# Performance work log

Hardware: AMD Instinct MI355X
Metric: run time of the kernel (lower is better)

The kernel has to match this reference:

```python
import jax, jax.numpy as jnp
import numpy as np

B, C, HEADS, W, Hh = 8, 512, 8, 32, 32
D = C // HEADS  # 64 per-head dim
N = W * Hh      # 1024 spatial tokens


def setup_inputs() -> dict:
    key = jax.random.key(0)
    ks = jax.random.split(key, 10)
    s = 1.0 / np.sqrt(C)
    return {
        "x": jax.random.normal(ks[0], (B, C, W, Hh), dtype=jnp.float32),
        "Wq": jax.random.normal(ks[1], (C, C), dtype=jnp.float32) * s,
        "bq": jax.random.normal(ks[2], (C,), dtype=jnp.float32) * 0.01,
        "Wk": jax.random.normal(ks[3], (C, C), dtype=jnp.float32) * s,
        "bk": jax.random.normal(ks[4], (C,), dtype=jnp.float32) * 0.01,
        "Wv": jax.random.normal(ks[5], (C, C), dtype=jnp.float32) * s,
        "bv": jax.random.normal(ks[6], (C,), dtype=jnp.float32) * 0.01,
        "rel_h": jax.random.normal(ks[7], (1, HEADS, D, 1, Hh), dtype=jnp.float32),
        "rel_w": jax.random.normal(ks[8], (1, HEADS, D, W, 1), dtype=jnp.float32),
    }


def reference(x, Wq, bq, Wk, bk, Wv, bv, rel_h, rel_w):
    b = x.shape[0]
    xf = x.reshape(b, C, N)  # [B, C, N] — 1x1 conv == per-position linear
    proj = lambda Wm, bm: (jnp.einsum('oc,bcn->bon', Wm, xf) + bm[None, :, None]).reshape(b, HEADS, D, N)
    q = proj(Wq, bq)  # [B, H, D, N]
    k = proj(Wk, bk)
    v = proj(Wv, bv)
    # content-content: q^T k -> [B, H, N, N]
    cc = jnp.einsum('bhdn,bhdm->bhnm', q, k)
    # relative position bias: (rel_h + rel_w) -> [H, D, N], then rel^T @ q
    rel = (rel_h + rel_w).reshape(HEADS, D, N)
    cp = jnp.einsum('hdn,bhdm->bhnm', rel, q)  # [B, H, N, N]
    attn = jax.nn.softmax(cc + cp, axis=-1)
    # out = v @ attn^T : out[d,m] = sum_n v[d,n] * attn[m,n]
    out = jnp.einsum('bhdn,bhmn->bhdm', v, attn)  # [B, H, D, N]
    return out.reshape(b, C, W, Hh)
```

## Files before the change

kernel.cpp:

```cpp
#include <hip/hip_runtime.h>

typedef _Float16 half8 __attribute__((ext_vector_type(8)));
typedef _Float16 half4 __attribute__((ext_vector_type(4)));
typedef float f32x4 __attribute__((ext_vector_type(4)));

__device__ __forceinline__ void glds16(const void* g, void* l) {
    __builtin_amdgcn_global_load_lds(
        (const __attribute__((address_space(1))) unsigned int*)g,
        (__attribute__((address_space(3))) unsigned int*)l, 16, 0, 0);
}


__global__ void k_prep_all(const float* __restrict__ Wq, const float* __restrict__ Wk,
                           const float* __restrict__ Wv, const float* __restrict__ bq,
                           const float* __restrict__ bk, const float* __restrict__ bv,
                           const float* __restrict__ x, const float* __restrict__ rel_h,
                           const float* __restrict__ rel_w, _Float16* __restrict__ Wf,
                           float* __restrict__ bias2, _Float16* __restrict__ xTf,
                           _Float16* __restrict__ rel2) {
    __shared__ float xs[64][65];
    int bid = blockIdx.x;
    if (bid < 384) {
        int t = bid * 256 + threadIdx.x;
        int m = t >> 6;
        int c8 = (t & 63) << 3;
        const float* src = (m < 512) ? (Wq + m * 512)
                         : (m < 1024 ? (Wk + (m - 512) * 512) : (Wv + (m - 1024) * 512));
        float4 v0 = *(const float4*)(src + c8);
        float4 v1 = *(const float4*)(src + c8 + 4);
        half8 o;
        o[0] = (_Float16)v0.x; o[1] = (_Float16)v0.y; o[2] = (_Float16)v0.z; o[3] = (_Float16)v0.w;
        o[4] = (_Float16)v1.x; o[5] = (_Float16)v1.y; o[6] = (_Float16)v1.z; o[7] = (_Float16)v1.w;
        *(half8*)(Wf + (size_t)m * 512 + c8) = o;
        if (t < 1536)
            bias2[t] = (t < 512) ? bq[t] : (t < 1024 ? bk[t - 512] : bv[t - 1024]);
    } else if (bid < 1408) {
        int i = bid - 384;
        int nt = (i & 15) << 6, ct = ((i >> 4) & 7) << 6, b = i >> 7;
        int t = threadIdx.x;
        const float* xb = x + ((size_t)b * 512 + ct) * 1024 + nt;
#pragma unroll
        for (int p = 0; p < 4; ++p) {
            int c = p * 16 + (t >> 4), n4 = (t & 15) * 4;
            float4 v = *(const float4*)(xb + (size_t)c * 1024 + n4);
            xs[c][n4] = v.x; xs[c][n4 + 1] = v.y; xs[c][n4 + 2] = v.z; xs[c][n4 + 3] = v.w;
        }
        __syncthreads();
        int nl = t >> 2, part = t & 3;
        _Float16* rowp = xTf + ((size_t)b * 1024 + nt + nl) * 512;
#pragma unroll
        for (int g = 0; g < 2; ++g) {
            half8 o;
#pragma unroll
            for (int j = 0; j < 8; ++j)
                o[j] = (_Float16)xs[part * 16 + g * 8 + j][nl];
            *(half8*)(rowp + ct + part * 16 + g * 8) = o;
        }
    } else {
        int tid = (bid - 1408) * 256 + threadIdx.x;
        int h = tid >> 13;
        int rem = tid & 8191;
        int n = rem >> 3;
        int g = rem & 7;
        int hh = n & 31, ww = n >> 5;
        half8 o;
#pragma unroll
        for (int j = 0; j < 8; ++j) {
            int d = g * 8 + j;
            o[j] = (_Float16)(rel_h[(h * 64 + d) * 32 + hh] + rel_w[(h * 64 + d) * 32 + ww]);
        }
        *(half8*)(rel2 + ((size_t)h * 1024 + n) * 64 + g * 8) = o;
    }
}

__global__ __launch_bounds__(256, 3) void k_proj(const _Float16* __restrict__ Wf,
                                                 const _Float16* __restrict__ xTf,
                                                 const float* __restrict__ bias2,
                                                 _Float16* __restrict__ q2,
                                                 _Float16* __restrict__ k2,
                                                 _Float16* __restrict__ vb) {
    __shared__ __align__(16) _Float16 As[8192];
    __shared__ __align__(16) _Float16 Bs[8192];
    int t = threadIdx.x;
    int lane = t & 63, w = t >> 6;
    int lm = lane & 15, lq = lane >> 4;
    int wr = (w >> 1) * 64, wc = (w & 1) * 64;
    int mb = blockIdx.y * 128, nb = blockIdx.x * 128, b = blockIdx.z;
    int rl = lane >> 2;
    int csw = ((lane & 3) ^ ((lane >> 3) & 3)) * 8;
    const _Float16* Ag0 = Wf + (size_t)(mb + w * 32 + rl) * 512 + csw;
    const _Float16* Ag1 = Ag0 + 16 * 512;
    const _Float16* Bg0 = xTf + ((size_t)b * 1024 + nb + w * 32 + rl) * 512 + csw;
    const _Float16* Bg1 = Bg0 + 16 * 512;
    f32x4 acc[4][4];
#pragma unroll
    for (int i = 0; i < 4; ++i)
#pragma unroll
        for (int j = 0; j < 4; ++j) acc[i][j] = {0.f, 0.f, 0.f, 0.f};
    int fsw = (lq ^ ((lm >> 1) & 3)) * 8;
    for (int k0 = 0; k0 < 512; k0 += 64) {
#pragma unroll
        for (int kh = 0; kh < 2; ++kh) {
            int ko = k0 + kh * 32;
            glds16(Ag0 + ko, &As[kh * 4096 + (w * 32) * 32]);
            glds16(Ag1 + ko, &As[kh * 4096 + (w * 32 + 16) * 32]);
            glds16(Bg0 + ko, &Bs[kh * 4096 + (w * 32) * 32]);
            glds16(Bg1 + ko, &Bs[kh * 4096 + (w * 32 + 16) * 32]);
        }
        __syncthreads();
#pragma unroll
        for (int kh = 0; kh < 2; ++kh) {
            half8 af[4], bfr[4];
#pragma unroll
            for (int mt = 0; mt < 4; ++mt)
                af[mt] = *(half8*)&As[kh * 4096 + (wr + mt * 16 + lm) * 32 + fsw];
#pragma unroll
            for (int nt = 0; nt < 4; ++nt)
                bfr[nt] = *(half8*)&Bs[kh * 4096 + (wc + nt * 16 + lm) * 32 + fsw];
#pragma unroll
            for (int mt = 0; mt < 4; ++mt)
#pragma unroll
                for (int nt = 0; nt < 4; ++nt)
                    acc[mt][nt] = __builtin_amdgcn_mfma_f32_16x16x32_f16(af[mt], bfr[nt], acc[mt][nt], 0, 0, 0);
        }
        __syncthreads();
    }
    int sect = mb >> 9;
    int hloc = ((mb & 511) + wr) >> 6;
    size_t bh = (size_t)b * 8 + hloc;
    if (sect < 2) {
        float sc = (sect == 0) ? 1.44269504089f : 1.0f;
        _Float16* dst = (sect == 0 ? q2 : k2) + bh * 1024 * 64;
#pragma unroll
        for (int mt = 0; mt < 4; ++mt) {
            int d0 = mt * 16 + lq * 4;
            float bi0 = bias2[mb + wr + d0];
            float bi1 = bias2[mb + wr + d0 + 1];
            float bi2 = bias2[mb + wr + d0 + 2];
            float bi3 = bias2[mb + wr + d0 + 3];
#pragma unroll
            for (int nt = 0; nt < 4; ++nt) {
                int n = nb + wc + nt * 16 + lm;
                half4 o;
                o[0] = (_Float16)((acc[mt][nt][0] + bi0) * sc);
                o[1] = (_Float16)((acc[mt][nt][1] + bi1) * sc);
                o[2] = (_Float16)((acc[mt][nt][2] + bi2) * sc);
                o[3] = (_Float16)((acc[mt][nt][3] + bi3) * sc);
                *(half4*)(dst + (size_t)n * 64 + d0) = o;
            }
        }
    } else {
        _Float16* dst = vb + bh * 64 * 1024;
#pragma unroll
        for (int mt = 0; mt < 4; ++mt)
#pragma unroll
            for (int reg = 0; reg < 4; ++reg) {
                int d = mt * 16 + lq * 4 + reg;
                float bi = bias2[mb + wr + d];
#pragma unroll
                for (int nt = 0; nt < 4; ++nt) {
                    int n = nb + wc + nt * 16 + lm;
                    dst[(size_t)d * 1024 + n] = (_Float16)(acc[mt][nt][reg] + bi);
                }
            }
    }
}

__global__ __launch_bounds__(256, 3) void k_attn(const _Float16* __restrict__ q2,
                                                 const _Float16* __restrict__ k2,
                                                 const _Float16* __restrict__ rel2,
                                                 const _Float16* __restrict__ vb,
                                                 float* __restrict__ out) {
    __shared__ __align__(16) char pool[45056];
    _Float16* kb_s = (_Float16*)pool;
    _Float16* v_s  = (_Float16*)(pool + 17408);
    _Float16* p_s  = (_Float16*)(pool + 26624);
    int t = threadIdx.x;
    int lane = t & 63, w = t >> 6;
    int lm = lane & 15, lq = lane >> 4;
    int lin = blockIdx.x;
    int mt0 = lin >> 6;
    int bh_ = lin & 63;
    int h = bh_ & 7, b = bh_ >> 3;
    size_t bh = (size_t)b * 8 + h;
    const _Float16* q2b = q2 + bh * 1024 * 64;
    const _Float16* k2b = k2 + bh * 1024 * 64;
    const _Float16* relb = rel2 + (size_t)h * 1024 * 64;
    const _Float16* vbb = vb + bh * 64 * 1024;
    float* outb = out + bh * 64 * 1024 + mt0 * 128;

    int r = t >> 2, part = t & 3;
    const _Float16* ksrc = ((part < 2) ? (k2b + part * 32) : (q2b + (part - 2) * 32));
    int vc = (t & 3) * 16;
    const _Float16* vsrcb = vbb + (size_t)r * 1024 + vc;
    _Float16* kdst = kb_s + r * 136 + part * 32;
    _Float16* vdst = v_s + r * 72 + vc;

    uint4 kc0, kc1, kc2, kc3, vv0, vv1;
    {
        const uint4* s_ = (const uint4*)(ksrc + (size_t)r * 64);
        kc0 = s_[0]; kc1 = s_[1]; kc2 = s_[2]; kc3 = s_[3];
        const uint4* v_ = (const uint4*)vsrcb;
        vv0 = v_[0]; vv1 = v_[1];
    }

    {
        int n = mt0 * 128 + r;
        const _Float16* src = (part < 2) ? (q2b + (size_t)n * 64 + part * 32)
                                         : (relb + (size_t)n * 64 + (part - 2) * 32);
        ((uint4*)kdst)[0] = ((const uint4*)src)[0];
        ((uint4*)kdst)[1] = ((const uint4*)src)[1];
        ((uint4*)kdst)[2] = ((const uint4*)src)[2];
        ((uint4*)kdst)[3] = ((const uint4*)src)[3];
    }
    __syncthreads();
    half8 ah0[4], ah1[4];
#pragma unroll
    for (int kk = 0; kk < 4; ++kk)
        ah0[kk] = *(half8*)&kb_s[(w * 16 + lm) * 136 + kk * 32 + lq * 8];
    __syncthreads();
    {
        int n = mt0 * 128 + 64 + r;
        const _Float16* src = (part < 2) ? (q2b + (size_t)n * 64 + part * 32)
                                         : (relb + (size_t)n * 64 + (part - 2) * 32);
        ((uint4*)kdst)[0] = ((const uint4*)src)[0];
        ((uint4*)kdst)[1] = ((const uint4*)src)[1];
        ((uint4*)kdst)[2] = ((const uint4*)src)[2];
        ((uint4*)kdst)[3] = ((const uint4*)src)[3];
    }
    __syncthreads();
#pragma unroll
    for (int kk = 0; kk < 4; ++kk)
        ah1[kk] = *(half8*)&kb_s[(w * 16 + lm) * 136 + kk * 32 + lq * 8];
    __syncthreads();

    f32x4 acco0[4], acco1[4];
#pragma unroll
    for (int i = 0; i < 4; ++i) { acco0[i] = {0.f, 0.f, 0.f, 0.f}; acco1[i] = {0.f, 0.f, 0.f, 0.f}; }
    float mrun0 = -3e38f, lrun0 = 0.f, mrun1 = -3e38f, lrun1 = 0.f;

    for (int kt = 0; kt < 16; ++kt) {
        ((uint4*)kdst)[0] = kc0;
        ((uint4*)kdst)[1] = kc1;
        ((uint4*)kdst)[2] = kc2;
        ((uint4*)kdst)[3] = kc3;
        ((uint4*)vdst)[0] = vv0;
        ((uint4*)vdst)[1] = vv1;
        __syncthreads();
        int nn = ((kt + 1) & 15) * 64;
        const uint4* s_ = (const uint4*)(ksrc + (size_t)(nn + r) * 64);
        uint4 kn0 = s_[0], kn1 = s_[1], kn2 = s_[2], kn3 = s_[3];
        const uint4* v_ = (const uint4*)(vsrcb + nn);
        uint4 vn0 = v_[0], vn1 = v_[1];
        f32x4 s0[4], s1[4];
#pragma unroll
        for (int ct = 0; ct < 4; ++ct) { s0[ct] = {0.f, 0.f, 0.f, 0.f}; s1[ct] = {0.f, 0.f, 0.f, 0.f}; }
#pragma unroll
        for (int ct = 0; ct < 4; ++ct) {
            half8 kf[4];
#pragma unroll
            for (int kk = 0; kk < 4; ++kk)
                kf[kk] = *(half8*)&kb_s[(ct * 16 + lm) * 136 + kk * 32 + lq * 8];
#pragma unroll
            for (int kk = 0; kk < 4; ++kk) {
                s0[ct] = __builtin_amdgcn_mfma_f32_16x16x32_f16(kf[kk], ah0[kk], s0[ct], 0, 0, 0);
                s1[ct] = __builtin_amdgcn_mfma_f32_16x16x32_f16(kf[kk], ah1[kk], s1[ct], 0, 0, 0);
            }
        }
        {
            float mx = -3e38f;
#pragma unroll
            for (int ct = 0; ct < 4; ++ct)
#pragma unroll
                for (int reg = 0; reg < 4; ++reg) mx = fmaxf(mx, s0[ct][reg]);
            mx = fmaxf(mx, __shfl_xor(mx, 16));
            mx = fmaxf(mx, __shfl_xor(mx, 32));
            float mnew = fmaxf(mrun0, mx);
            float al_ = exp2f(mrun0 - mnew);
            float rs = 0.f;
#pragma unroll
            for (int ct = 0; ct < 4; ++ct) {
                float p0 = exp2f(s0[ct][0] - mnew);
                float p1 = exp2f(s0[ct][1] - mnew);
                float p2 = exp2f(s0[ct][2] - mnew);
                float p3 = exp2f(s0[ct][3] - mnew);
                rs += (p0 + p1) + (p2 + p3);
                half4 o; o[0] = (_Float16)p0; o[1] = (_Float16)p1; o[2] = (_Float16)p2; o[3] = (_Float16)p3;
                *(half4*)&p_s[(w * 16 + lm) * 72 + ct * 16 + lq * 4] = o;
            }
            rs += __shfl_xor(rs, 16);
            rs += __shfl_xor(rs, 32);
            lrun0 = lrun0 * al_ + rs;
            mrun0 = mnew;
#pragma unroll
            for (int dt = 0; dt < 4; ++dt) {
                acco0[dt][0] *= al_; acco0[dt][1] *= al_;
                acco0[dt][2] *= al_; acco0[dt][3] *= al_;
            }
        }
        {
            float mx = -3e38f;
#pragma unroll
            for (int ct = 0; ct < 4; ++ct)
#pragma unroll
                for (int reg = 0; reg < 4; ++reg) mx = fmaxf(mx, s1[ct][reg]);
            mx = fmaxf(mx, __shfl_xor(mx, 16));
            mx = fmaxf(mx, __shfl_xor(mx, 32));
            float mnew = fmaxf(mrun1, mx);
            float al_ = exp2f(mrun1 - mnew);
            float rs = 0.f;
#pragma unroll
            for (int ct = 0; ct < 4; ++ct) {
                float p0 = exp2f(s1[ct][0] - mnew);
                float p1 = exp2f(s1[ct][1] - mnew);
                float p2 = exp2f(s1[ct][2] - mnew);
                float p3 = exp2f(s1[ct][3] - mnew);
                rs += (p0 + p1) + (p2 + p3);
                half4 o; o[0] = (_Float16)p0; o[1] = (_Float16)p1; o[2] = (_Float16)p2; o[3] = (_Float16)p3;
                *(half4*)&p_s[(64 + w * 16 + lm) * 72 + ct * 16 + lq * 4] = o;
            }
            rs += __shfl_xor(rs, 16);
            rs += __shfl_xor(rs, 32);
            lrun1 = lrun1 * al_ + rs;
            mrun1 = mnew;
#pragma unroll
            for (int dt = 0; dt < 4; ++dt) {
                acco1[dt][0] *= al_; acco1[dt][1] *= al_;
                acco1[dt][2] *= al_; acco1[dt][3] *= al_;
            }
        }
        half8 p0f[2], p1f[2];
#pragma unroll
        for (int ch = 0; ch < 2; ++ch) {
            p0f[ch] = *(half8*)&p_s[(w * 16 + lm) * 72 + ch * 32 + lq * 8];
            p1f[ch] = *(half8*)&p_s[(64 + w * 16 + lm) * 72 + ch * 32 + lq * 8];
        }
#pragma unroll
        for (int dt = 0; dt < 4; ++dt) {
            half8 vf0 = *(half8*)&v_s[(dt * 16 + lm) * 72 + lq * 8];
            half8 vf1 = *(half8*)&v_s[(dt * 16 + lm) * 72 + 32 + lq * 8];
            acco0[dt] = __builtin_amdgcn_mfma_f32_16x16x32_f16(vf0, p0f[0], acco0[dt], 0, 0, 0);
            acco0[dt] = __builtin_amdgcn_mfma_f32_16x16x32_f16(vf1, p0f[1], acco0[dt], 0, 0, 0);
            acco1[dt] = __builtin_amdgcn_mfma_f32_16x16x32_f16(vf0, p1f[0], acco1[dt], 0, 0, 0);
            acco1[dt] = __builtin_amdgcn_mfma_f32_16x16x32_f16(vf1, p1f[1], acco1[dt], 0, 0, 0);
        }
        __syncthreads();
        kc0 = kn0; kc1 = kn1; kc2 = kn2; kc3 = kn3;
        vv0 = vn0; vv1 = vn1;
    }
    float li0 = 1.f / lrun0, li1 = 1.f / lrun1;
#pragma unroll
    for (int dt = 0; dt < 4; ++dt)
#pragma unroll
        for (int reg = 0; reg < 4; ++reg) {
            int d = dt * 16 + lq * 4 + reg;
            outb[(size_t)d * 1024 + w * 16 + lm] = acco0[dt][reg] * li0;
            outb[(size_t)d * 1024 + 64 + w * 16 + lm] = acco1[dt][reg] * li1;
        }
}

extern "C" void kernel_launch(void* const* d_in, const int* in_sizes, int n_in,
                              void* d_out, int out_size, void* d_ws, size_t ws_size,
                              hipStream_t stream) {
    const float* x     = (const float*)d_in[0];
    const float* Wq    = (const float*)d_in[1];
    const float* bq    = (const float*)d_in[2];
    const float* Wk    = (const float*)d_in[3];
    const float* bk    = (const float*)d_in[4];
    const float* Wv    = (const float*)d_in[5];
    const float* bv    = (const float*)d_in[6];
    const float* rel_h = (const float*)d_in[7];
    const float* rel_w = (const float*)d_in[8];
    char* ws = (char*)d_ws;
    _Float16* Wf   = (_Float16*)(ws);
    float* bias2   = (float*)(ws + 1572864);
    _Float16* xTf  = (_Float16*)(ws + 1579008);
    _Float16* q2   = (_Float16*)(ws + 9967616);
    _Float16* k2   = (_Float16*)(ws + 18356224);
    _Float16* vb   = (_Float16*)(ws + 26744832);
    _Float16* rel2 = (_Float16*)(ws + 35133440);
    float* out = (float*)d_out;

    hipLaunchKernelGGL(k_prep_all, dim3(1664),     dim3(256), 0, stream,
                       Wq, Wk, Wv, bq, bk, bv, x, rel_h, rel_w, Wf, bias2, xTf, rel2);
    hipLaunchKernelGGL(k_proj,     dim3(8, 12, 8), dim3(256), 0, stream, Wf, xTf, bias2, q2, k2, vb);
    hipLaunchKernelGGL(k_attn,     dim3(512),      dim3(256), 0, stream, q2, k2, rel2, vb, out);
}
```

Before: 153.6 us.

## Fuse prep and projection kernels via persistent grid with global atomic barrier

Merges the input-conversion kernel and the QKV projection GEMM into one launch of 768 blocks. Each block first handles a grid-stride share of the prep work, then all blocks wait on a global atomic counter barrier before running the projection tile. This removes a kernel launch and its inter-kernel gap. In exchange it adds a memset per call and relies on all 768 blocks being co-resident (256 CUs × 3 blocks), otherwise the barrier deadlocks.

After: 262.2 us. 70.6% more time.

```diff
diff --git a/kernel.cpp b/kernel.cpp
--- a/kernel.cpp
+++ b/kernel.cpp
@@ -11,158 +11,176 @@
 }
 
 
-__global__ void k_prep_all(const float* __restrict__ Wq, const float* __restrict__ Wk,
-                           const float* __restrict__ Wv, const float* __restrict__ bq,
-                           const float* __restrict__ bk, const float* __restrict__ bv,
-                           const float* __restrict__ x, const float* __restrict__ rel_h,
-                           const float* __restrict__ rel_w, _Float16* __restrict__ Wf,
-                           float* __restrict__ bias2, _Float16* __restrict__ xTf,
-                           _Float16* __restrict__ rel2) {
-    __shared__ float xs[64][65];
-    int bid = blockIdx.x;
-    if (bid < 384) {
-        int t = bid * 256 + threadIdx.x;
-        int m = t >> 6;
-        int c8 = (t & 63) << 3;
-        const float* src = (m < 512) ? (Wq + m * 512)
-                         : (m < 1024 ? (Wk + (m - 512) * 512) : (Wv + (m - 1024) * 512));
-        float4 v0 = *(const float4*)(src + c8);
-        float4 v1 = *(const float4*)(src + c8 + 4);
-        half8 o;
-        o[0] = (_Float16)v0.x; o[1] = (_Float16)v0.y; o[2] = (_Float16)v0.z; o[3] = (_Float16)v0.w;
-        o[4] = (_Float16)v1.x; o[5] = (_Float16)v1.y; o[6] = (_Float16)v1.z; o[7] = (_Float16)v1.w;
-        *(half8*)(Wf + (size_t)m * 512 + c8) = o;
-        if (t < 1536)
-            bias2[t] = (t < 512) ? bq[t] : (t < 1024 ? bk[t - 512] : bv[t - 1024]);
-    } else if (bid < 1408) {
-        int i = bid - 384;
-        int nt = (i & 15) << 6, ct = ((i >> 4) & 7) << 6, b = i >> 7;
+__global__ __launch_bounds__(256, 3) void k_prep_proj(
+    const float* __restrict__ Wq, const float* __restrict__ Wk,
+    const float* __restrict__ Wv, const float* __restrict__ bq,
+    const float* __restrict__ bk, const float* __restrict__ bv,
+    const float* __restrict__ x, const float* __restrict__ rel_h,
+    const float* __restrict__ rel_w, _Float16* __restrict__ Wf,
+    float* __restrict__ bias2, _Float16* __restrict__ xTf,
+    _Float16* __restrict__ rel2, _Float16* __restrict__ q2,
+    _Float16* __restrict__ k2, _Float16* __restrict__ vb,
+    unsigned int* __restrict__ bar) {
+    __shared__ __align__(16) char smem[32768];
+
+    for (int vbid = blockIdx.x; vbid < 1664; vbid += 768) {
+        if (vbid < 384) {
+            int t = vbid * 256 + threadIdx.x;
+            int m = t >> 6;
+            int c8 = (t & 63) << 3;
+            const float* src = (m < 512) ? (Wq + m * 512)
+                             : (m < 1024 ? (Wk + (m - 512) * 512) : (Wv + (m - 1024) * 512));
+            float4 v0 = *(const float4*)(src + c8);
+            float4 v1 = *(const float4*)(src + c8 + 4);
+            half8 o;
+            o[0] = (_Float16)v0.x; o[1] = (_Float16)v0.y; o[2] = (_Float16)v0.z; o[3] = (_Float16)v0.w;
+            o[4] = (_Float16)v1.x; o[5] = (_Float16)v1.y; o[6] = (_Float16)v1.z; o[7] = (_Float16)v1.w;
+            *(half8*)(Wf + (size_t)m * 512 + c8) = o;
+            if (t < 1536)
+                bias2[t] = (t < 512) ? bq[t] : (t < 1024 ? bk[t - 512] : bv[t - 1024]);
+        } else if (vbid < 1408) {
+            float (*xs)[65] = (float(*)[65])smem;
+            int i = vbid - 384;
+            int nt = (i & 15) << 6, ct = ((i >> 4) & 7) << 6, b = i >> 7;
+            int t = threadIdx.x;
+            const float* xb = x + ((size_t)b * 512 + ct) * 1024 + nt;
+#pragma unroll
+            for (int p = 0; p < 4; ++p) {
+                int c = p * 16 + (t >> 4), n4 = (t & 15) * 4;
+                float4 v = *(const float4*)(xb + (size_t)c * 1024 + n4);
+                xs[c][n4] = v.x; xs[c][n4 + 1] = v.y; xs[c][n4 + 2] = v.z; xs[c][n4 + 3] = v.w;
+            }
+            __syncthreads();
+            int nl = t >> 2, part = t & 3;
+            _Float16* rowp = xTf + ((size_t)b * 1024 + nt + nl) * 512;
+#pragma unroll
+            for (int g = 0; g < 2; ++g) {
+                half8 o;
+#pragma unroll
+                for (int j = 0; j < 8; ++j)
+                    o[j] = (_Float16)xs[part * 16 + g * 8 + j][nl];
+                *(half8*)(rowp + ct + part * 16 + g * 8) = o;
+            }
+        } else {
+            int tid = (vbid - 1408) * 256 + threadIdx.x;
+            int h = tid >> 13;
+            int rem = tid & 8191;
+            int n = rem >> 3;
+            int g = rem & 7;
+            int hh = n & 31, ww = n >> 5;
+            half8 o;
+#pragma unroll
+            for (int j = 0; j < 8; ++j) {
+                int d = g * 8 + j;
+                o[j] = (_Float16)(rel_h[(h * 64 + d) * 32 + hh] + rel_w[(h * 64 + d) * 32 + ww]);
+            }
+            *(half8*)(rel2 + ((size_t)h * 1024 + n) * 64 + g * 8) = o;
+        }
+        __syncthreads();
+    }
+
+    __syncthreads();
+    if (threadIdx.x == 0) {
+        __threadfence();
+        __hip_atomic_fetch_add(bar, 1u, __ATOMIC_RELEASE, __HIP_MEMORY_SCOPE_AGENT);
+        unsigned int v;
+        do {
+            __builtin_amdgcn_s_sleep(8);
+            v = __hip_atomic_load(bar, __ATOMIC_ACQUIRE, __HIP_MEMORY_SCOPE_AGENT);
+        } while (v < 768u);
+        __threadfence();
+    }
+    __syncthreads();
+
+    _Float16* As = (_Float16*)smem;
+    _Float16* Bs = (_Float16*)(smem + 16384);
+    {
         int t = threadIdx.x;
-        const float* xb = x + ((size_t)b * 512 + ct) * 1024 + nt;
-#pragma unroll
-        for (int p = 0; p < 4; ++p) {
-            int c = p * 16 + (t >> 4), n4 = (t & 15) * 4;
-            float4 v = *(const float4*)(xb + (size_t)c * 1024 + n4);
-            xs[c][n4] = v.x; xs[c][n4 + 1] = v.y; xs[c][n4 + 2] = v.z; xs[c][n4 + 3] = v.w;
-        }
-        __syncthreads();
-        int nl = t >> 2, part = t & 3;
-        _Float16* rowp = xTf + ((size_t)b * 1024 + nt + nl) * 512;
-#pragma unroll
-        for (int g = 0; g < 2; ++g) {
-            half8 o;
-#pragma unroll
-            for (int j = 0; j < 8; ++j)
-                o[j] = (_Float16)xs[part * 16 + g * 8 + j][nl];
-            *(half8*)(rowp + ct + part * 16 + g * 8) = o;
-        }
-    } else {
-        int tid = (bid - 1408) * 256 + threadIdx.x;
-        int h = tid >> 13;
-        int rem = tid & 8191;
-        int n = rem >> 3;
-        int g = rem & 7;
-        int hh = n & 31, ww = n >> 5;
-        half8 o;
-#pragma unroll
-        for (int j = 0; j < 8; ++j) {
-            int d = g * 8 + j;
-            o[j] = (_Float16)(rel_h[(h * 64 + d) * 32 + hh] + rel_w[(h * 64 + d) * 32 + ww]);
-        }
-        *(half8*)(rel2 + ((size_t)h * 1024 + n) * 64 + g * 8) = o;
-    }
-}
-
-__global__ __launch_bounds__(256, 3) void k_proj(const _Float16* __restrict__ Wf,
-                                                 const _Float16* __restrict__ xTf,
-                                                 const float* __restrict__ bias2,
-                                                 _Float16* __restrict__ q2,
-                                                 _Float16* __restrict__ k2,
-                                                 _Float16* __restrict__ vb) {
-    __shared__ __align__(16) _Float16 As[8192];
-    __shared__ __align__(16) _Float16 Bs[8192];
-    int t = threadIdx.x;
-    int lane = t & 63, w = t >> 6;
-    int lm = lane & 15, lq = lane >> 4;
-    int wr = (w >> 1) * 64, wc = (w & 1) * 64;
-    int mb = blockIdx.y * 128, nb = blockIdx.x * 128, b = blockIdx.z;
-    int rl = lane >> 2;
-    int csw = ((lane & 3) ^ ((lane >> 3) & 3)) * 8;
-    const _Float16* Ag0 = Wf + (size_t)(mb + w * 32 + rl) * 512 + csw;
-    const _Float16* Ag1 = Ag0 + 16 * 512;
-    const _Float16* Bg0 = xTf + ((size_t)b * 1024 + nb + w * 32 + rl) * 512 + csw;
-    const _Float16* Bg1 = Bg0 + 16 * 512;
-    f32x4 acc[4][4];
-#pragma unroll
-    for (int i = 0; i < 4; ++i)
-#pragma unroll
-        for (int j = 0; j < 4; ++j) acc[i][j] = {0.f, 0.f, 0.f, 0.f};
-    int fsw = (lq ^ ((lm >> 1) & 3)) * 8;
-    for (int k0 = 0; k0 < 512; k0 += 64) {
-#pragma unroll
-        for (int kh = 0; kh < 2; ++kh) {
-            int ko = k0 + kh * 32;
-            glds16(Ag0 + ko, &As[kh * 4096 + (w * 32) * 32]);
-            glds16(Ag1 + ko, &As[kh * 4096 + (w * 32 + 16) * 32]);
-            glds16(Bg0 + ko, &Bs[kh * 4096 + (w * 32) * 32]);
-            glds16(Bg1 + ko, &Bs[kh * 4096 + (w * 32 + 16) * 32]);
-        }
-        __syncthreads();
-#pragma unroll
-        for (int kh = 0; kh < 2; ++kh) {
-            half8 af[4], bfr[4];
-#pragma unroll
-            for (int mt = 0; mt < 4; ++mt)
-                af[mt] = *(half8*)&As[kh * 4096 + (wr + mt * 16 + lm) * 32 + fsw];
-#pragma unroll
-            for (int nt = 0; nt < 4; ++nt)
-                bfr[nt] = *(half8*)&Bs[kh * 4096 + (wc + nt * 16 + lm) * 32 + fsw];
-#pragma unroll
-            for (int mt = 0; mt < 4; ++mt)
+        int lane = t & 63, w = t >> 6;
+        int lm = lane & 15, lq = lane >> 4;
+        int wr = (w >> 1) * 64, wc = (w & 1) * 64;
+        int bid = blockIdx.x;
+        int b = bid & 7;
+        int rest = bid >> 3;
+        int mb = (rest % 12) * 128, nb = (rest / 12) * 128;
+        int rl = lane >> 2;
+        int csw = ((lane & 3) ^ ((lane >> 3) & 3)) * 8;
+        const _Float16* Ag0 = Wf + (size_t)(mb + w * 32 + rl) * 512 + csw;
+        const _Float16* Ag1 = Ag0 + 16 * 512;
+        const _Float16* Bg0 = xTf + ((size_t)b * 1024 + nb + w * 32 + rl) * 512 + csw;
+        const _Float16* Bg1 = Bg0 + 16 * 512;
+        f32x4 acc[4][4];
+#pragma unroll
+        for (int i = 0; i < 4; ++i)
+#pragma unroll
+            for (int j = 0; j < 4; ++j) acc[i][j] = {0.f, 0.f, 0.f, 0.f};
+        int fsw = (lq ^ ((lm >> 1) & 3)) * 8;
+        for (int k0 = 0; k0 < 512; k0 += 64) {
+#pragma unroll
+            for (int kh = 0; kh < 2; ++kh) {
+                int ko = k0 + kh * 32;
+                glds16(Ag0 + ko, &As[kh * 4096 + (w * 32) * 32]);
+                glds16(Ag1 + ko, &As[kh * 4096 + (w * 32 + 16) * 32]);
+                glds16(Bg0 + ko, &Bs[kh * 4096 + (w * 32) * 32]);
+                glds16(Bg1 + ko, &Bs[kh * 4096 + (w * 32 + 16) * 32]);
+            }
+            __syncthreads();
+#pragma unroll
+            for (int kh = 0; kh < 2; ++kh) {
+                half8 af[4], bfr[4];
+#pragma unroll
+                for (int mt = 0; mt < 4; ++mt)
+                    af[mt] = *(half8*)&As[kh * 4096 + (wr + mt * 16 + lm) * 32 + fsw];
 #pragma unroll
                 for (int nt = 0; nt < 4; ++nt)
-                    acc[mt][nt] = __builtin_amdgcn_mfma_f32_16x16x32_f16(af[mt], bfr[nt], acc[mt][nt], 0, 0, 0);
-        }
-        __syncthreads();
-    }
-    int sect = mb >> 9;
-    int hloc = ((mb & 511) + wr) >> 6;
-    size_t bh = (size_t)b * 8 + hloc;
-    if (sect < 2) {
-        float sc = (sect == 0) ? 1.44269504089f : 1.0f;
-        _Float16* dst = (sect == 0 ? q2 : k2) + bh * 1024 * 64;
-#pragma unroll
-        for (int mt = 0; mt < 4; ++mt) {
-            int d0 = mt * 16 + lq * 4;
-            float bi0 = bias2[mb + wr + d0];
-            float bi1 = bias2[mb + wr + d0 + 1];
-            float bi2 = bias2[mb + wr + d0 + 2];
-            float bi3 = bias2[mb + wr + d0 + 3];
-#pragma unroll
-            for (int nt = 0; nt < 4; ++nt) {
-                int n = nb + wc + nt * 16 + lm;
-                half4 o;
-                o[0] = (_Float16)((acc[mt][nt][0] + bi0) * sc);
-                o[1] = (_Float16)((acc[mt][nt][1] + bi1) * sc);
-                o[2] = (_Float16)((acc[mt][nt][2] + bi2) * sc);
-                o[3] = (_Float16)((acc[mt][nt][3] + bi3) * sc);
-                *(half4*)(dst + (size_t)n * 64 + d0) = o;
-            }
-        }
-    } else {
-        _Float16* dst = vb + bh * 64 * 1024;
-#pragma unroll
-        for (int mt = 0; mt < 4; ++mt)
-#pragma unroll
-            for (int reg = 0; reg < 4; ++reg) {
-                int d = mt * 16 + lq * 4 + reg;
-                float bi = bias2[mb + wr + d];
+                    bfr[nt] = *(half8*)&Bs[kh * 4096 + (wc + nt * 16 + lm) * 32 + fsw];
+#pragma unroll
+                for (int mt = 0; mt < 4; ++mt)
+#pragma unroll
+                    for (int nt = 0; nt < 4; ++nt)
+                        acc[mt][nt] = __builtin_amdgcn_mfma_f32_16x16x32_f16(af[mt], bfr[nt], acc[mt][nt], 0, 0, 0);
+            }
+            __syncthreads();
+        }
+        int sect = mb >> 9;
+        int hloc = ((mb & 511) + wr) >> 6;
+        size_t bh = (size_t)b * 8 + hloc;
+        if (sect < 2) {
+            float sc = (sect == 0) ? 1.44269504089f : 1.0f;
+            _Float16* dst = (sect == 0 ? q2 : k2) + bh * 1024 * 64;
+#pragma unroll
+            for (int mt = 0; mt < 4; ++mt) {
+                int d0 = mt * 16 + lq * 4;
+                float bi0 = bias2[mb + wr + d0];
+                float bi1 = bias2[mb + wr + d0 + 1];
+                float bi2 = bias2[mb + wr + d0 + 2];
+                float bi3 = bias2[mb + wr + d0 + 3];
 #pragma unroll
                 for (int nt = 0; nt < 4; ++nt) {
                     int n = nb + wc + nt * 16 + lm;
-                    dst[(size_t)d * 1024 + n] = (_Float16)(acc[mt][nt][reg] + bi);
+                    half4 o;
+                    o[0] = (_Float16)((acc[mt][nt][0] + bi0) * sc);
+                    o[1] = (_Float16)((acc[mt][nt][1] + bi1) * sc);
+                    o[2] = (_Float16)((acc[mt][nt][2] + bi2) * sc);
+                    o[3] = (_Float16)((acc[mt][nt][3] + bi3) * sc);
+                    *(half4*)(dst + (size_t)n * 64 + d0) = o;
                 }
             }
+        } else {
+            _Float16* dst = vb + bh * 64 * 1024;
+#pragma unroll
+            for (int mt = 0; mt < 4; ++mt)
+#pragma unroll
+                for (int reg = 0; reg < 4; ++reg) {
+                    int d = mt * 16 + lq * 4 + reg;
+                    float bi = bias2[mb + wr + d];
+#pragma unroll
+                    for (int nt = 0; nt < 4; ++nt) {
+                        int n = nb + wc + nt * 16 + lm;
+                        dst[(size_t)d * 1024 + n] = (_Float16)(acc[mt][nt][reg] + bi);
+                    }
+                }
+        }
     }
 }
 
@@ -379,10 +397,12 @@
     _Float16* k2   = (_Float16*)(ws + 18356224);
     _Float16* vb   = (_Float16*)(ws + 26744832);
     _Float16* rel2 = (_Float16*)(ws + 35133440);
+    unsigned int* bar = (unsigned int*)(ws + 36182016);
     float* out = (float*)d_out;
 
-    hipLaunchKernelGGL(k_prep_all, dim3(1664),     dim3(256), 0, stream,
-                       Wq, Wk, Wv, bq, bk, bv, x, rel_h, rel_w, Wf, bias2, xTf, rel2);
-    hipLaunchKernelGGL(k_proj,     dim3(8, 12, 8), dim3(256), 0, stream, Wf, xTf, bias2, q2, k2, vb);
-    hipLaunchKernelGGL(k_attn,     dim3(512),      dim3(256), 0, stream, q2, k2, rel2, vb, out);
+    hipMemsetAsync(bar, 0, 64, stream);
+    hipLaunchKernelGGL(k_prep_proj, dim3(768), dim3(256), 0, stream,
+                       Wq, Wk, Wv, bq, bk, bv, x, rel_h, rel_w,
+                       Wf, bias2, xTf, rel2, q2, k2, vb, bar);
+    hipLaunchKernelGGL(k_attn, dim3(512), dim3(256), 0, stream, q2, k2, rel2, vb, out);
 }
```

## Fuse x transpose and fp16 conversion into the projection GEMM load

Applied to the files above, without the earlier changes.

Drops the separate pass that transposed x into an fp16 [B,N,C] workspace buffer. The projection kernel now reads fp32 x directly, converts it to fp16 in registers, and writes it transposed into padded, swizzled shared memory. This saves a full write and re-read of the 8 MB intermediate and shrinks the prep kernel. In exchange, B-tile loads become synchronous register loads instead of async global-to-LDS copies, the GEMM reads twice as many bytes for x, and the grid is reordered so batch is the fastest axis.

After: 158.3 us. +3.0%, slower.

```diff
diff --git a/kernel.cpp b/kernel.cpp
--- a/kernel.cpp
+++ b/kernel.cpp
@@ -11,14 +11,12 @@
 }
 
 
-__global__ void k_prep_all(const float* __restrict__ Wq, const float* __restrict__ Wk,
-                           const float* __restrict__ Wv, const float* __restrict__ bq,
-                           const float* __restrict__ bk, const float* __restrict__ bv,
-                           const float* __restrict__ x, const float* __restrict__ rel_h,
-                           const float* __restrict__ rel_w, _Float16* __restrict__ Wf,
-                           float* __restrict__ bias2, _Float16* __restrict__ xTf,
-                           _Float16* __restrict__ rel2) {
-    __shared__ float xs[64][65];
+__global__ void k_prep_wrel(const float* __restrict__ Wq, const float* __restrict__ Wk,
+                            const float* __restrict__ Wv, const float* __restrict__ bq,
+                            const float* __restrict__ bk, const float* __restrict__ bv,
+                            const float* __restrict__ rel_h, const float* __restrict__ rel_w,
+                            _Float16* __restrict__ Wf, float* __restrict__ bias2,
+                            _Float16* __restrict__ rel2) {
     int bid = blockIdx.x;
     if (bid < 384) {
         int t = bid * 256 + threadIdx.x;
@@ -34,30 +32,8 @@
         *(half8*)(Wf + (size_t)m * 512 + c8) = o;
         if (t < 1536)
             bias2[t] = (t < 512) ? bq[t] : (t < 1024 ? bk[t - 512] : bv[t - 1024]);
-    } else if (bid < 1408) {
-        int i = bid - 384;
-        int nt = (i & 15) << 6, ct = ((i >> 4) & 7) << 6, b = i >> 7;
-        int t = threadIdx.x;
-        const float* xb = x + ((size_t)b * 512 + ct) * 1024 + nt;
-#pragma unroll
-        for (int p = 0; p < 4; ++p) {
-            int c = p * 16 + (t >> 4), n4 = (t & 15) * 4;
-            float4 v = *(const float4*)(xb + (size_t)c * 1024 + n4);
-            xs[c][n4] = v.x; xs[c][n4 + 1] = v.y; xs[c][n4 + 2] = v.z; xs[c][n4 + 3] = v.w;
-        }
-        __syncthreads();
-        int nl = t >> 2, part = t & 3;
-        _Float16* rowp = xTf + ((size_t)b * 1024 + nt + nl) * 512;
-#pragma unroll
-        for (int g = 0; g < 2; ++g) {
-            half8 o;
-#pragma unroll
-            for (int j = 0; j < 8; ++j)
-                o[j] = (_Float16)xs[part * 16 + g * 8 + j][nl];
-            *(half8*)(rowp + ct + part * 16 + g * 8) = o;
-        }
     } else {
-        int tid = (bid - 1408) * 256 + threadIdx.x;
+        int tid = (bid - 384) * 256 + threadIdx.x;
         int h = tid >> 13;
         int rem = tid & 8191;
         int n = rem >> 3;
@@ -73,25 +49,26 @@
     }
 }
 
-__global__ __launch_bounds__(256, 3) void k_proj(const _Float16* __restrict__ Wf,
-                                                 const _Float16* __restrict__ xTf,
-                                                 const float* __restrict__ bias2,
-                                                 _Float16* __restrict__ q2,
-                                                 _Float16* __restrict__ k2,
-                                                 _Float16* __restrict__ vb) {
+__global__ __launch_bounds__(256, 3) void k_projx(const _Float16* __restrict__ Wf,
+                                                  const float* __restrict__ x,
+                                                  const float* __restrict__ bias2,
+                                                  _Float16* __restrict__ q2,
+                                                  _Float16* __restrict__ k2,
+                                                  _Float16* __restrict__ vb) {
     __shared__ __align__(16) _Float16 As[8192];
-    __shared__ __align__(16) _Float16 Bs[8192];
+    __shared__ __align__(16) _Float16 Bs[10240];
     int t = threadIdx.x;
     int lane = t & 63, w = t >> 6;
     int lm = lane & 15, lq = lane >> 4;
     int wr = (w >> 1) * 64, wc = (w & 1) * 64;
-    int mb = blockIdx.y * 128, nb = blockIdx.x * 128, b = blockIdx.z;
+    int mb = blockIdx.y * 128, nb = blockIdx.z * 128, b = blockIdx.x;
     int rl = lane >> 2;
     int csw = ((lane & 3) ^ ((lane >> 3) & 3)) * 8;
     const _Float16* Ag0 = Wf + (size_t)(mb + w * 32 + rl) * 512 + csw;
     const _Float16* Ag1 = Ag0 + 16 * 512;
-    const _Float16* Bg0 = xTf + ((size_t)b * 1024 + nb + w * 32 + rl) * 512 + csw;
-    const _Float16* Bg1 = Bg0 + 16 * 512;
+    int nq = t & 31;
+    int cqb = t >> 5;
+    const float* xbase = x + (size_t)b * 512 * 1024 + nb + nq * 4;
     f32x4 acc[4][4];
 #pragma unroll
     for (int i = 0; i < 4; ++i)
@@ -104,8 +81,33 @@
             int ko = k0 + kh * 32;
             glds16(Ag0 + ko, &As[kh * 4096 + (w * 32) * 32]);
             glds16(Ag1 + ko, &As[kh * 4096 + (w * 32 + 16) * 32]);
-            glds16(Bg0 + ko, &Bs[kh * 4096 + (w * 32) * 32]);
-            glds16(Bg1 + ko, &Bs[kh * 4096 + (w * 32 + 16) * 32]);
+        }
+#pragma unroll
+        for (int s = 0; s < 2; ++s) {
+            int cq = cqb + s * 8;
+            int c0 = cq * 4;
+            const float* xp = xbase + (size_t)(k0 + c0) * 1024;
+            float4 f0 = *(const float4*)(xp);
+            float4 f1 = *(const float4*)(xp + 1024);
+            float4 f2 = *(const float4*)(xp + 2048);
+            float4 f3 = *(const float4*)(xp + 3072);
+            int kh = c0 >> 5;
+            int col32 = c0 & 31;
+            _Float16* bsh = &Bs[kh * 5120];
+#pragma unroll
+            for (int j = 0; j < 4; ++j) {
+                int jj = (j + nq) & 3;
+                float e0 = (jj == 0) ? f0.x : (jj == 1) ? f0.y : (jj == 2) ? f0.z : f0.w;
+                float e1 = (jj == 0) ? f1.x : (jj == 1) ? f1.y : (jj == 2) ? f1.z : f1.w;
+                float e2 = (jj == 0) ? f2.x : (jj == 1) ? f2.y : (jj == 2) ? f2.z : f2.w;
+                float e3 = (jj == 0) ? f3.x : (jj == 1) ? f3.y : (jj == 2) ? f3.z : f3.w;
+                int row = nq * 4 + jj;
+                int colx = col32 ^ (((row >> 4) & 3) << 3);
+                half4 hv;
+                hv[0] = (_Float16)e0; hv[1] = (_Float16)e1;
+                hv[2] = (_Float16)e2; hv[3] = (_Float16)e3;
+                *(half4*)&bsh[row * 40 + colx] = hv;
+            }
         }
         __syncthreads();
 #pragma unroll
@@ -116,7 +118,7 @@
                 af[mt] = *(half8*)&As[kh * 4096 + (wr + mt * 16 + lm) * 32 + fsw];
 #pragma unroll
             for (int nt = 0; nt < 4; ++nt)
-                bfr[nt] = *(half8*)&Bs[kh * 4096 + (wc + nt * 16 + lm) * 32 + fsw];
+                bfr[nt] = *(half8*)&Bs[kh * 5120 + (wc + nt * 16 + lm) * 40 + ((lq * 8) ^ (nt << 3))];
 #pragma unroll
             for (int mt = 0; mt < 4; ++mt)
 #pragma unroll
@@ -374,15 +376,14 @@
     char* ws = (char*)d_ws;
     _Float16* Wf   = (_Float16*)(ws);
     float* bias2   = (float*)(ws + 1572864);
-    _Float16* xTf  = (_Float16*)(ws + 1579008);
-    _Float16* q2   = (_Float16*)(ws + 9967616);
-    _Float16* k2   = (_Float16*)(ws + 18356224);
-    _Float16* vb   = (_Float16*)(ws + 26744832);
-    _Float16* rel2 = (_Float16*)(ws + 35133440);
+    _Float16* q2   = (_Float16*)(ws + 1579008);
+    _Float16* k2   = (_Float16*)(ws + 9967616);
+    _Float16* vb   = (_Float16*)(ws + 18356224);
+    _Float16* rel2 = (_Float16*)(ws + 26744832);
     float* out = (float*)d_out;
 
-    hipLaunchKernelGGL(k_prep_all, dim3(1664),     dim3(256), 0, stream,
-                       Wq, Wk, Wv, bq, bk, bv, x, rel_h, rel_w, Wf, bias2, xTf, rel2);
-    hipLaunchKernelGGL(k_proj,     dim3(8, 12, 8), dim3(256), 0, stream, Wf, xTf, bias2, q2, k2, vb);
-    hipLaunchKernelGGL(k_attn,     dim3(512),      dim3(256), 0, stream, q2, k2, rel2, vb, out);
-}
+    hipLaunchKernelGGL(k_prep_wrel, dim3(640),      dim3(256), 0, stream,
+                       Wq, Wk, Wv, bq, bk, bv, rel_h, rel_w, Wf, bias2, rel2);
+    hipLaunchKernelGGL(k_projx,     dim3(8, 12, 8), dim3(256), 0, stream, Wf, x, bias2, q2, k2, vb);
+    hipLaunchKernelGGL(k_attn,      dim3(512),      dim3(256), 0, stream, q2, k2, rel2, vb, out);
+}
```

## Fuse fp32-to-fp16 conversion and transpose into projection GEMM tile loads

Applied to the files above, without the earlier changes.

Removes the separate prep kernel that converted W and x to fp16 and transposed x. The projection GEMM now reads fp32 W and x directly, converts them in registers and writes padded (stride 40) LDS tiles. The rel table build is folded into the same launch as extra blocks. This drops one launch and the round trip of fp16 intermediates through memory, at the cost of twice the global bytes per tile load, no async global-to-LDS loads, and W being re-converted by every block that uses it.

New measurement: 168.8 us. 1.1x slower.

```diff
diff --git a/kernel.cpp b/kernel.cpp
--- a/kernel.cpp
+++ b/kernel.cpp
@@ -4,60 +4,22 @@
 typedef _Float16 half4 __attribute__((ext_vector_type(4)));
 typedef float f32x4 __attribute__((ext_vector_type(4)));
 
-__device__ __forceinline__ void glds16(const void* g, void* l) {
-    __builtin_amdgcn_global_load_lds(
-        (const __attribute__((address_space(1))) unsigned int*)g,
-        (__attribute__((address_space(3))) unsigned int*)l, 16, 0, 0);
-}
-
-
-__global__ void k_prep_all(const float* __restrict__ Wq, const float* __restrict__ Wk,
-                           const float* __restrict__ Wv, const float* __restrict__ bq,
-                           const float* __restrict__ bk, const float* __restrict__ bv,
-                           const float* __restrict__ x, const float* __restrict__ rel_h,
-                           const float* __restrict__ rel_w, _Float16* __restrict__ Wf,
-                           float* __restrict__ bias2, _Float16* __restrict__ xTf,
-                           _Float16* __restrict__ rel2) {
-    __shared__ float xs[64][65];
+
+__global__ __launch_bounds__(256, 3) void k_proj_all(
+    const float* __restrict__ Wq, const float* __restrict__ Wk,
+    const float* __restrict__ Wv, const float* __restrict__ bq,
+    const float* __restrict__ bk, const float* __restrict__ bv,
+    const float* __restrict__ x, const float* __restrict__ rel_h,
+    const float* __restrict__ rel_w, _Float16* __restrict__ q2,
+    _Float16* __restrict__ k2, _Float16* __restrict__ vb,
+    _Float16* __restrict__ rel2) {
+    __shared__ __align__(16) _Float16 As[2 * 128 * 40];
+    __shared__ __align__(16) _Float16 Bs[2 * 128 * 40];
     int bid = blockIdx.x;
-    if (bid < 384) {
-        int t = bid * 256 + threadIdx.x;
-        int m = t >> 6;
-        int c8 = (t & 63) << 3;
-        const float* src = (m < 512) ? (Wq + m * 512)
-                         : (m < 1024 ? (Wk + (m - 512) * 512) : (Wv + (m - 1024) * 512));
-        float4 v0 = *(const float4*)(src + c8);
-        float4 v1 = *(const float4*)(src + c8 + 4);
-        half8 o;
-        o[0] = (_Float16)v0.x; o[1] = (_Float16)v0.y; o[2] = (_Float16)v0.z; o[3] = (_Float16)v0.w;
-        o[4] = (_Float16)v1.x; o[5] = (_Float16)v1.y; o[6] = (_Float16)v1.z; o[7] = (_Float16)v1.w;
-        *(half8*)(Wf + (size_t)m * 512 + c8) = o;
-        if (t < 1536)
-            bias2[t] = (t < 512) ? bq[t] : (t < 1024 ? bk[t - 512] : bv[t - 1024]);
-    } else if (bid < 1408) {
-        int i = bid - 384;
-        int nt = (i & 15) << 6, ct = ((i >> 4) & 7) << 6, b = i >> 7;
-        int t = threadIdx.x;
-        const float* xb = x + ((size_t)b * 512 + ct) * 1024 + nt;
-#pragma unroll
-        for (int p = 0; p < 4; ++p) {
-            int c = p * 16 + (t >> 4), n4 = (t & 15) * 4;
-            float4 v = *(const float4*)(xb + (size_t)c * 1024 + n4);
-            xs[c][n4] = v.x; xs[c][n4 + 1] = v.y; xs[c][n4 + 2] = v.z; xs[c][n4 + 3] = v.w;
-        }
-        __syncthreads();
-        int nl = t >> 2, part = t & 3;
-        _Float16* rowp = xTf + ((size_t)b * 1024 + nt + nl) * 512;
-#pragma unroll
-        for (int g = 0; g < 2; ++g) {
-            half8 o;
-#pragma unroll
-            for (int j = 0; j < 8; ++j)
-                o[j] = (_Float16)xs[part * 16 + g * 8 + j][nl];
-            *(half8*)(rowp + ct + part * 16 + g * 8) = o;
-        }
-    } else {
-        int tid = (bid - 1408) * 256 + threadIdx.x;
+    int t = threadIdx.x;
+
+    if (bid >= 768) {
+        int tid = (bid - 768) * 256 + t;
         int h = tid >> 13;
         int rem = tid & 8191;
         int n = rem >> 3;
@@ -70,42 +32,76 @@
             o[j] = (_Float16)(rel_h[(h * 64 + d) * 32 + hh] + rel_w[(h * 64 + d) * 32 + ww]);
         }
         *(half8*)(rel2 + ((size_t)h * 1024 + n) * 64 + g * 8) = o;
-    }
-}
-
-__global__ __launch_bounds__(256, 3) void k_proj(const _Float16* __restrict__ Wf,
-                                                 const _Float16* __restrict__ xTf,
-                                                 const float* __restrict__ bias2,
-                                                 _Float16* __restrict__ q2,
-                                                 _Float16* __restrict__ k2,
-                                                 _Float16* __restrict__ vb) {
-    __shared__ __align__(16) _Float16 As[8192];
-    __shared__ __align__(16) _Float16 Bs[8192];
-    int t = threadIdx.x;
+        return;
+    }
+
     int lane = t & 63, w = t >> 6;
     int lm = lane & 15, lq = lane >> 4;
     int wr = (w >> 1) * 64, wc = (w & 1) * 64;
-    int mb = blockIdx.y * 128, nb = blockIdx.x * 128, b = blockIdx.z;
-    int rl = lane >> 2;
-    int csw = ((lane & 3) ^ ((lane >> 3) & 3)) * 8;
-    const _Float16* Ag0 = Wf + (size_t)(mb + w * 32 + rl) * 512 + csw;
-    const _Float16* Ag1 = Ag0 + 16 * 512;
-    const _Float16* Bg0 = xTf + ((size_t)b * 1024 + nb + w * 32 + rl) * 512 + csw;
-    const _Float16* Bg1 = Bg0 + 16 * 512;
+    int b = bid & 7;
+    int rest = bid >> 3;
+    int mb = (rest % 12) * 128, nb = (rest / 12) * 128;
+    int msel = mb >> 9;
+    int mrow0 = mb & 511;
+    const float* Wsel = (msel == 0) ? Wq : ((msel == 1) ? Wk : Wv);
+
+    int am = t >> 1;
+    int akh = t & 1;
+    const float* wrow = Wsel + (size_t)(mrow0 + am) * 512 + akh * 32;
+    int nq = t & 31;
+    int ch = t >> 5;
+    int bkh = ch >> 2;
+    int c32 = (ch & 3) * 8;
+    const float* xrow = x + (size_t)b * 512 * 1024 + nb + nq * 4;
+
     f32x4 acc[4][4];
 #pragma unroll
     for (int i = 0; i < 4; ++i)
 #pragma unroll
         for (int j = 0; j < 4; ++j) acc[i][j] = {0.f, 0.f, 0.f, 0.f};
-    int fsw = (lq ^ ((lm >> 1) & 3)) * 8;
+
     for (int k0 = 0; k0 < 512; k0 += 64) {
-#pragma unroll
-        for (int kh = 0; kh < 2; ++kh) {
-            int ko = k0 + kh * 32;
-            glds16(Ag0 + ko, &As[kh * 4096 + (w * 32) * 32]);
-            glds16(Ag1 + ko, &As[kh * 4096 + (w * 32 + 16) * 32]);
-            glds16(Bg0 + ko, &Bs[kh * 4096 + (w * 32) * 32]);
-            glds16(Bg1 + ko, &Bs[kh * 4096 + (w * 32 + 16) * 32]);
+        {
+            const float* wp = wrow + k0;
+            float4 wf[8];
+#pragma unroll
+            for (int i = 0; i < 8; ++i) wf[i] = ((const float4*)wp)[i];
+            _Float16* arow = &As[akh * 5120 + am * 40];
+#pragma unroll
+            for (int q = 0; q < 2; ++q) {
+                half8 h;
+                h[0] = (_Float16)wf[q * 4 + 0].x; h[1] = (_Float16)wf[q * 4 + 0].y;
+                h[2] = (_Float16)wf[q * 4 + 0].z; h[3] = (_Float16)wf[q * 4 + 0].w;
+                h[4] = (_Float16)wf[q * 4 + 1].x; h[5] = (_Float16)wf[q * 4 + 1].y;
+                h[6] = (_Float16)wf[q * 4 + 1].z; h[7] = (_Float16)wf[q * 4 + 1].w;
+                half8 h2;
+                h2[0] = (_Float16)wf[q * 4 + 2].x; h2[1] = (_Float16)wf[q * 4 + 2].y;
+                h2[2] = (_Float16)wf[q * 4 + 2].z; h2[3] = (_Float16)wf[q * 4 + 2].w;
+                h2[4] = (_Float16)wf[q * 4 + 3].x; h2[5] = (_Float16)wf[q * 4 + 3].y;
+                h2[6] = (_Float16)wf[q * 4 + 3].z; h2[7] = (_Float16)wf[q * 4 + 3].w;
+                *(half8*)(arow + q * 16) = h;
+                *(half8*)(arow + q * 16 + 8) = h2;
+            }
+        }
+        {
+            const float* xp = xrow + (size_t)(k0 + ch * 8) * 1024;
+            float4 xf[8];
+#pragma unroll
+            for (int i = 0; i < 8; ++i) xf[i] = *(const float4*)(xp + (size_t)i * 1024);
+            _Float16* bbase = &Bs[bkh * 5120 + c32];
+#pragma unroll
+            for (int j = 0; j < 4; ++j) {
+                half8 h;
+                h[0] = (_Float16)((const float*)&xf[0])[j];
+                h[1] = (_Float16)((const float*)&xf[1])[j];
+                h[2] = (_Float16)((const float*)&xf[2])[j];
+                h[3] = (_Float16)((const float*)&xf[3])[j];
+                h[4] = (_Float16)((const float*)&xf[4])[j];
+                h[5] = (_Float16)((const float*)&xf[5])[j];
+                h[6] = (_Float16)((const float*)&xf[6])[j];
+                h[7] = (_Float16)((const float*)&xf[7])[j];
+                *(half8*)(bbase + (nq * 4 + j) * 40) = h;
+            }
         }
         __syncthreads();
 #pragma unroll
@@ -113,10 +109,10 @@
             half8 af[4], bfr[4];
 #pragma unroll
             for (int mt = 0; mt < 4; ++mt)
-                af[mt] = *(half8*)&As[kh * 4096 + (wr + mt * 16 + lm) * 32 + fsw];
+                af[mt] = *(half8*)&As[kh * 5120 + (wr + mt * 16 + lm) * 40 + lq * 8];
 #pragma unroll
             for (int nt = 0; nt < 4; ++nt)
-                bfr[nt] = *(half8*)&Bs[kh * 4096 + (wc + nt * 16 + lm) * 32 + fsw];
+                bfr[nt] = *(half8*)&Bs[kh * 5120 + (wc + nt * 16 + lm) * 40 + lq * 8];
 #pragma unroll
             for (int mt = 0; mt < 4; ++mt)
 #pragma unroll
@@ -125,19 +121,19 @@
         }
         __syncthreads();
     }
-    int sect = mb >> 9;
-    int hloc = ((mb & 511) + wr) >> 6;
+    const float* bsel = (msel == 0) ? bq : ((msel == 1) ? bk : bv);
+    int hloc = (mrow0 + wr) >> 6;
     size_t bh = (size_t)b * 8 + hloc;
-    if (sect < 2) {
-        float sc = (sect == 0) ? 1.44269504089f : 1.0f;
-        _Float16* dst = (sect == 0 ? q2 : k2) + bh * 1024 * 64;
+    if (msel < 2) {
+        float sc = (msel == 0) ? 1.44269504089f : 1.0f;
+        _Float16* dst = (msel == 0 ? q2 : k2) + bh * 1024 * 64;
 #pragma unroll
         for (int mt = 0; mt < 4; ++mt) {
             int d0 = mt * 16 + lq * 4;
-            float bi0 = bias2[mb + wr + d0];
-            float bi1 = bias2[mb + wr + d0 + 1];
-            float bi2 = bias2[mb + wr + d0 + 2];
-            float bi3 = bias2[mb + wr + d0 + 3];
+            float bi0 = bsel[mrow0 + wr + d0];
+            float bi1 = bsel[mrow0 + wr + d0 + 1];
+            float bi2 = bsel[mrow0 + wr + d0 + 2];
+            float bi3 = bsel[mrow0 + wr + d0 + 3];
 #pragma unroll
             for (int nt = 0; nt < 4; ++nt) {
                 int n = nb + wc + nt * 16 + lm;
@@ -156,7 +152,7 @@
 #pragma unroll
             for (int reg = 0; reg < 4; ++reg) {
                 int d = mt * 16 + lq * 4 + reg;
-                float bi = bias2[mb + wr + d];
+                float bi = bsel[mrow0 + wr + d];
 #pragma unroll
                 for (int nt = 0; nt < 4; ++nt) {
                     int n = nb + wc + nt * 16 + lm;
@@ -372,17 +368,13 @@
     const float* rel_h = (const float*)d_in[7];
     const float* rel_w = (const float*)d_in[8];
     char* ws = (char*)d_ws;
-    _Float16* Wf   = (_Float16*)(ws);
-    float* bias2   = (float*)(ws + 1572864);
-    _Float16* xTf  = (_Float16*)(ws + 1579008);
-    _Float16* q2   = (_Float16*)(ws + 9967616);
-    _Float16* k2   = (_Float16*)(ws + 18356224);
-    _Float16* vb   = (_Float16*)(ws + 26744832);
-    _Float16* rel2 = (_Float16*)(ws + 35133440);
+    _Float16* q2   = (_Float16*)(ws);
+    _Float16* k2   = (_Float16*)(ws + 8388608);
+    _Float16* vb   = (_Float16*)(ws + 16777216);
+    _Float16* rel2 = (_Float16*)(ws + 25165824);
     float* out = (float*)d_out;
 
-    hipLaunchKernelGGL(k_prep_all, dim3(1664),     dim3(256), 0, stream,
-                       Wq, Wk, Wv, bq, bk, bv, x, rel_h, rel_w, Wf, bias2, xTf, rel2);
-    hipLaunchKernelGGL(k_proj,     dim3(8, 12, 8), dim3(256), 0, stream, Wf, xTf, bias2, q2, k2, vb);
-    hipLaunchKernelGGL(k_attn,     dim3(512),      dim3(256), 0, stream, q2, k2, rel2, vb, out);
+    hipLaunchKernelGGL(k_proj_all, dim3(1024), dim3(256), 0, stream,
+                       Wq, Wk, Wv, bq, bk, bv, x, rel_h, rel_w, q2, k2, vb, rel2);
+    hipLaunchKernelGGL(k_attn,     dim3(512),  dim3(256), 0, stream, q2, k2, rel2, vb, out);
 }
```
